# Performance work log

Hardware: AMD Instinct MI355X
Metric: run time of the kernel (lower is better)

The kernel has to match this reference:

```python
import jax, jax.numpy as jnp
import numpy as np

B, S, HID = 2, 1024, 2048
NH, NKV = 32, 8
HD = HID // NH          # 64
N_REP = NH // NKV       # 4
ROPE_BASE = 10000.0


def rope_tables(seq_len, dim):
    inv_freq = 1.0 / (ROPE_BASE ** (np.arange(0, dim, 2, dtype=np.float32) / dim))
    t = jnp.arange(seq_len, dtype=jnp.float32)
    freqs = jnp.outer(t, jnp.asarray(inv_freq))          # [S, HD/2]
    emb = jnp.concatenate([freqs, freqs], axis=-1)       # [S, HD]
    return jnp.cos(emb), jnp.sin(emb)


def rotate_half(x):
    half = x.shape[-1] // 2
    return jnp.concatenate([-x[..., half:], x[..., :half]], axis=-1)


def setup_inputs() -> dict:
    key = jax.random.key(0)
    k1, k2, k3, k4, k5 = jax.random.split(key, 5)
    hidden_states = jax.random.normal(k1, (B, S, HID), dtype=jnp.float32)
    position_ids = jnp.broadcast_to(jnp.arange(S, dtype=jnp.int32), (B, S))
    # additive causal mask [B,1,S,S]: 0 where allowed, large negative where masked
    neg = jnp.finfo(jnp.float32).min
    causal = jnp.tril(jnp.ones((S, S), dtype=bool))
    attention_mask = jnp.where(causal, 0.0, neg)[None, None].astype(jnp.float32)
    attention_mask = jnp.broadcast_to(attention_mask, (B, 1, S, S))
    scale = 0.02
    Wq = jax.random.normal(k2, (HID, NH * HD), dtype=jnp.float32) * scale
    Wk = jax.random.normal(k3, (HID, NKV * HD), dtype=jnp.float32) * scale
    Wv = jax.random.normal(k4, (HID, NKV * HD), dtype=jnp.float32) * scale
    Wo = jax.random.normal(k5, (HID, HID), dtype=jnp.float32) * scale
    return {"hidden_states": hidden_states, "position_ids": position_ids,
            "attention_mask": attention_mask, "Wq": Wq, "Wk": Wk, "Wv": Wv, "Wo": Wo}


def reference(hidden_states, position_ids, attention_mask, Wq, Wk, Wv, Wo):
    b, s, _ = hidden_states.shape
    q = (hidden_states @ Wq).reshape(b, s, NH, HD).transpose(0, 2, 1, 3)    # [b,H,s,d]
    k = (hidden_states @ Wk).reshape(b, s, NKV, HD).transpose(0, 2, 1, 3)   # [b,kv,s,d]
    v = (hidden_states @ Wv).reshape(b, s, NKV, HD).transpose(0, 2, 1, 3)

    cos_t, sin_t = rope_tables(s, HD)                    # [s, d]
    cos = cos_t[position_ids][:, None]                   # [b,1,s,d]
    sin = sin_t[position_ids][:, None]
    q = q * cos + rotate_half(q) * sin
    k = k * cos + rotate_half(k) * sin

    # GQA: repeat each kv head N_REP times along the head axis
    k = jnp.repeat(k, N_REP, axis=1)                     # [b,H,s,d]
    v = jnp.repeat(v, N_REP, axis=1)

    scale = 1.0 / jnp.sqrt(jnp.asarray(HD, dtype=q.dtype))
    scores = jnp.einsum('bhqd,bhkd->bhqk', q, k) * scale
    scores = scores + attention_mask
    scores = jnp.maximum(scores, jnp.finfo(scores.dtype).min)
    w = jax.nn.softmax(scores, axis=-1)
    out = jnp.einsum('bhqk,bhkd->bhqd', w, v)            # [b,H,s,d]
    out = out.transpose(0, 2, 1, 3).reshape(b, s, HID)
    return out @ Wo
```

## Files before the change

### kernel.cpp

```cpp
#include <hip/hip_runtime.h>
#include <hip/hip_bf16.h>
#include <math.h>

constexpr int BB   = 2;
constexpr int SS   = 1024;
constexpr int HID  = 2048;
constexpr int NH   = 32;
constexpr int NKV  = 8;
constexpr int HD   = 64;
constexpr int M    = BB * SS;
constexpr int NQKV = 3072;

typedef __attribute__((ext_vector_type(8))) short bf8v;
typedef __attribute__((ext_vector_type(4))) float f4v;

static __device__ __forceinline__ unsigned short f2b(float x) {
  __hip_bfloat16 h = __float2bfloat16(x);
  return *reinterpret_cast<unsigned short*>(&h);
}
static __device__ __forceinline__ void gload16(void* lds, const void* g) {
  __builtin_amdgcn_global_load_lds(
      (const __attribute__((address_space(1))) void*)g,
      (__attribute__((address_space(3))) void*)lds, 16, 0, 0);
}

__global__ __launch_bounds__(256) void prepAll(
    const float* __restrict__ Wq, const float* __restrict__ Wk,
    const float* __restrict__ Wv, const float* __restrict__ Wo,
    const float* __restrict__ hidden, const int* __restrict__ pos_ids,
    unsigned short* __restrict__ WqkvT, unsigned short* __restrict__ WoT,
    unsigned short* __restrict__ Xb, float2* __restrict__ tab) {
  const int z = blockIdx.z;
  const int t = threadIdx.x;

  if (z == 4) {
    const int idx = blockIdx.y * 32 + blockIdx.x;
    if ((t & 127) < 32) {
      const int m = idx * 2 + (t >> 7);
      const int j = t & 31;
      const float pos = (float)pos_ids[m];
      const float ang = pos * exp2f(-(float)j * (13.287712379549449f / 32.0f));
      float sn, cs;
      sincosf(ang, &sn, &cs);
      tab[(size_t)m * 32 + j] = make_float2(cs, sn);
    }
    return;
  }
  if (z == 5) {
    const size_t base = ((size_t)(blockIdx.y * 32 + blockIdx.x)) * 4096;
#pragma unroll
    for (int it = 0; it < 2; ++it) {
      const size_t i = base + it * 2048 + t * 8;
      const float4 v0 = *(const float4*)(hidden + i);
      const float4 v1 = *(const float4*)(hidden + i + 4);
      unsigned short o[8] = {f2b(v0.x), f2b(v0.y), f2b(v0.z), f2b(v0.w),
                             f2b(v1.x), f2b(v1.y), f2b(v1.z), f2b(v1.w)};
      *(bf8v*)(Xb + i) = *(bf8v*)o;
    }
    return;
  }

  const float* src;
  unsigned short* dst;
  int C;
  if (z == 0)      { src = Wq; dst = WqkvT;                      C = 2048; }
  else if (z == 1) { src = Wk; dst = WqkvT + (size_t)2048 * HID; C = 512;  }
  else if (z == 2) { src = Wv; dst = WqkvT + (size_t)2560 * HID; C = 512;  }
  else             { src = Wo; dst = WoT;                        C = 2048; }

  const int r0 = blockIdx.y * 64, c0 = blockIdx.x * 64;
  if (c0 >= C) return;
  __shared__ float T[64][65];
  {
    const int r  = t >> 2;
    const int c4 = (t & 3) * 16;
    const float* sp = src + (size_t)(r0 + r) * C + c0 + c4;
    *(float4*)&T[r][c4 + 0]  = *(const float4*)(sp + 0);
    *(float4*)&T[r][c4 + 4]  = *(const float4*)(sp + 4);
    *(float4*)&T[r][c4 + 8]  = *(const float4*)(sp + 8);
    *(float4*)&T[r][c4 + 12] = *(const float4*)(sp + 12);
  }
  __syncthreads();
  {
    const int c  = t >> 2;
    const int rr = (t & 3) * 16;
    unsigned short o[16];
#pragma unroll
    for (int i = 0; i < 16; ++i) o[i] = f2b(T[rr + i][c]);
    unsigned short* dp = dst + (size_t)(c0 + c) * HID + r0 + rr;
    *(bf8v*)dp       = *(bf8v*)&o[0];
    *(bf8v*)(dp + 8) = *(bf8v*)&o[8];
  }
}


__global__ __launch_bounds__(512) void gemm_qkv(
    const unsigned short* __restrict__ A, const unsigned short* __restrict__ Bt,
    const float2* __restrict__ tab,
    unsigned short* __restrict__ Qb, unsigned short* __restrict__ Kb,
    unsigned short* __restrict__ Vt) {
  __shared__ unsigned short As[4][64 * 32];
  __shared__ unsigned short Bs[4][128 * 32];
  const int t  = threadIdx.x;
  const int w  = t >> 6, l = t & 63;
  const int lr = l & 15, lg = l >> 4;
  const int wr = w >> 1, wc = w & 1;
  const int bm = blockIdx.y * 64, bn = blockIdx.x * 128;

  f4v acc[4] = {};

  const unsigned short* Ablk = A  + (size_t)bm * HID;
  const unsigned short* Bblk = Bt + (size_t)bn * HID;
  const int srow = l >> 2;
  const int scol = (((l & 3) ^ ((srow >> 1) & 3)) * 8);
  const int rsl  = (lg ^ ((lr >> 1) & 3)) * 8;

  auto stageSS = [&](int u) {
    const int b0 = (u & 1) * 2;
    const int k0 = u * 64;
    if (w < 4) {
      gload16(&As[b0][(w * 16) * 32],     Ablk + (size_t)(w * 16 + srow) * HID + k0 + scol);
      gload16(&As[b0 + 1][(w * 16) * 32], Ablk + (size_t)(w * 16 + srow) * HID + k0 + 32 + scol);
      gload16(&Bs[b0][(w * 16) * 32],     Bblk + (size_t)(w * 16 + srow) * HID + k0 + scol);
      gload16(&Bs[b0 + 1][(w * 16) * 32], Bblk + (size_t)(w * 16 + srow) * HID + k0 + 32 + scol);
    } else {
      gload16(&Bs[b0][(w * 16) * 32],     Bblk + (size_t)(w * 16 + srow) * HID + k0 + scol);
      gload16(&Bs[b0 + 1][(w * 16) * 32], Bblk + (size_t)(w * 16 + srow) * HID + k0 + 32 + scol);
    }
  };

  const int nss = HID / 64;
  stageSS(0);
  asm volatile("s_waitcnt vmcnt(0)" ::: "memory");
  __builtin_amdgcn_s_barrier();

  const int aoff = (wr * 16 + lr) * 32 + rsl;
  const int boff = (wc * 64 + lr) * 32 + rsl;
  for (int u = 0; u < nss; ++u) {
    if (u + 1 < nss) stageSS(u + 1);
    const int b0 = (u & 1) * 2;

#pragma unroll
    for (int hlf = 0; hlf < 2; ++hlf) {
      const int cb = b0 + hlf;
      bf8v aF = *(const bf8v*)&As[cb][aoff];
      bf8v bF[4];
#pragma unroll
      for (int j = 0; j < 4; ++j)
        bF[j] = *(const bf8v*)&Bs[cb][boff + j * 512];
      __builtin_amdgcn_s_setprio(1);
#pragma unroll
      for (int ni = 0; ni < 4; ++ni)
        acc[ni] = __builtin_amdgcn_mfma_f32_16x16x32_bf16(aF, bF[ni], acc[ni], 0, 0, 0);
      __builtin_amdgcn_s_setprio(0);
    }

    asm volatile("s_waitcnt vmcnt(0)" ::: "memory");
    __builtin_amdgcn_s_barrier();
  }

  const int row0 = bm + wr * 16;
  const int colHead = bn + wc * 64;
  int mode, hh;
  if (colHead < 2048)      { mode = 0; hh = colHead >> 6;          }
  else if (colHead < 2560) { mode = 1; hh = (colHead - 2048) >> 6; }
  else                     { mode = 2; hh = (colHead - 2560) >> 6; }

#pragma unroll
  for (int r = 0; r < 4; ++r) {
    const int rowg = row0 + lg * 4 + r;
    const int bI = rowg >> 10, s = rowg & (SS - 1);
    if (mode == 2) {
      unsigned short* base = Vt + ((size_t)(bI * NKV + hh) * 64) * SS + s;
#pragma unroll
      for (int ni = 0; ni < 4; ++ni)
        base[(size_t)(ni * 16 + lr) * SS] = f2b(acc[ni][r]);
    } else {
      unsigned short* dst = (mode == 0)
          ? Qb + ((size_t)(bI * NH  + hh) * SS + s) * 64
          : Kb + ((size_t)(bI * NKV + hh) * SS + s) * 64;
      const float2 cs_lo = tab[(size_t)rowg * 32 + lr];
      const float2 cs_hi = tab[(size_t)rowg * 32 + 16 + lr];
#pragma unroll
      for (int ni = 0; ni < 4; ++ni) {
        const float2 cs = (ni & 1) ? cs_hi : cs_lo;
        const float x   = acc[ni][r];
        const float prt = acc[ni ^ 2][r];
        const float rh  = (ni < 2) ? -prt : prt;
        float v = x * cs.x + rh * cs.y;
        if (mode == 0) v *= 0.125f;
        dst[ni * 16 + lr] = f2b(v);
      }
    }
  }
}

__global__ __launch_bounds__(512) void gemm_bf16(
    const unsigned short* __restrict__ A, const unsigned short* __restrict__ Bt,
    float* __restrict__ C, int Ndim) {
  __shared__ unsigned short As[4][64 * 32];
  __shared__ unsigned short Bs[4][128 * 32];
  const int t  = threadIdx.x;
  const int w  = t >> 6, l = t & 63;
  const int lr = l & 15, lg = l >> 4;
  const int wr = w >> 1, wc = w & 1;
  const int bm = blockIdx.y * 64, bn = blockIdx.x * 128;

  f4v acc[4] = {};

  const unsigned short* Ablk = A  + (size_t)bm * HID;
  const unsigned short* Bblk = Bt + (size_t)bn * HID;
  const int srow = l >> 2;
  const int scol = (((l & 3) ^ ((srow >> 1) & 3)) * 8);
  const int rsl  = (lg ^ ((lr >> 1) & 3)) * 8;

  auto stageSS = [&](int u) {
    const int b0 = (u & 1) * 2;
    const int k0 = u * 64;
    if (w < 4) {
      gload16(&As[b0][(w * 16) * 32],     Ablk + (size_t)(w * 16 + srow) * HID + k0 + scol);
      gload16(&As[b0 + 1][(w * 16) * 32], Ablk + (size_t)(w * 16 + srow) * HID + k0 + 32 + scol);
      gload16(&Bs[b0][(w * 16) * 32],     Bblk + (size_t)(w * 16 + srow) * HID + k0 + scol);
      gload16(&Bs[b0 + 1][(w * 16) * 32], Bblk + (size_t)(w * 16 + srow) * HID + k0 + 32 + scol);
    } else {
      gload16(&Bs[b0][(w * 16) * 32],     Bblk + (size_t)(w * 16 + srow) * HID + k0 + scol);
      gload16(&Bs[b0 + 1][(w * 16) * 32], Bblk + (size_t)(w * 16 + srow) * HID + k0 + 32 + scol);
    }
  };

  const int nss = HID / 64;
  stageSS(0);
  asm volatile("s_waitcnt vmcnt(0)" ::: "memory");
  __builtin_amdgcn_s_barrier();

  const int aoff = (wr * 16 + lr) * 32 + rsl;
  const int boff = (wc * 64 + lr) * 32 + rsl;
  for (int u = 0; u < nss; ++u) {
    if (u + 1 < nss) stageSS(u + 1);
    const int b0 = (u & 1) * 2;

#pragma unroll
    for (int hlf = 0; hlf < 2; ++hlf) {
      const int cb = b0 + hlf;
      bf8v aF = *(const bf8v*)&As[cb][aoff];
      bf8v bF[4];
#pragma unroll
      for (int j = 0; j < 4; ++j)
        bF[j] = *(const bf8v*)&Bs[cb][boff + j * 512];
      __builtin_amdgcn_s_setprio(1);
#pragma unroll
      for (int ni = 0; ni < 4; ++ni)
        acc[ni] = __builtin_amdgcn_mfma_f32_16x16x32_bf16(aF, bF[ni], acc[ni], 0, 0, 0);
      __builtin_amdgcn_s_setprio(0);
    }

    asm volatile("s_waitcnt vmcnt(0)" ::: "memory");
    __builtin_amdgcn_s_barrier();
  }

  const int row0 = bm + wr * 16;
  const int col0 = bn + wc * 64;
#pragma unroll
  for (int r = 0; r < 4; ++r) {
    const size_t rowoff = (size_t)(row0 + lg * 4 + r) * Ndim;
#pragma unroll
    for (int ni = 0; ni < 4; ++ni)
      C[rowoff + col0 + ni * 16 + lr] = acc[ni][r];
  }
}

__global__ __launch_bounds__(128) void attn_mfma(
    const unsigned short* __restrict__ Qb, const unsigned short* __restrict__ Kb,
    const unsigned short* __restrict__ Vt, unsigned short* __restrict__ attn) {
  const int xb = blockIdx.x;
  const int h = blockIdx.y, b = blockIdx.z;
  const int kv = h >> 2;
  const int w  = threadIdx.x >> 6;
  const int l  = threadIdx.x & 63;
  const int lr = l & 15;
  const int lg = l >> 4;
  const int t  = threadIdx.x;

  __shared__ unsigned short VT[64][72];
  __shared__ unsigned short PL[2][16][72];

  const unsigned short* Kp = Kb + ((size_t)((b * NKV + kv) * SS)) * 64;
  const unsigned short* Vp = Vt + ((size_t)((b * NKV + kv) * 64)) * SS;

  const int vd  = t >> 1;
  const int vso = (t & 1) * 32;

  for (int half = 0; half < 2; ++half) {
    const int qt = half ? (31 - xb) : xb;
    const int qbase = qt * 32;
    const int qW = qbase + w * 16;
    const unsigned short* Qp = Qb + ((size_t)((b * NH + h) * SS + qW)) * 64;
    bf8v aQ0 = *(const bf8v*)(Qp + (size_t)lr * 64 + lg * 8);
    bf8v aQ1 = *(const bf8v*)(Qp + (size_t)lr * 64 + 32 + lg * 8);

    f4v o[4] = {{0,0,0,0},{0,0,0,0},{0,0,0,0},{0,0,0,0}};
    float lsumL[4] = {0.f, 0.f, 0.f, 0.f};

    bf8v kc[8];
#pragma unroll
    for (int c = 0; c < 4; ++c) {
      const unsigned short* kr = Kp + (size_t)(c * 16 + lr) * 64 + lg * 8;
      kc[2 * c]     = *(const bf8v*)(kr);
      kc[2 * c + 1] = *(const bf8v*)(kr + 32);
    }

    for (int kvb = 0; kvb < qbase + 32; kvb += 64) {
      __syncthreads();
      const unsigned short* vp = Vp + (size_t)vd * SS + kvb + vso;
      const bf8v v0 = *(const bf8v*)(vp);
      const bf8v v1 = *(const bf8v*)(vp + 8);
      const bf8v v2 = *(const bf8v*)(vp + 16);
      const bf8v v3 = *(const bf8v*)(vp + 24);

      f4v sc[4] = {{0,0,0,0},{0,0,0,0},{0,0,0,0},{0,0,0,0}};
      __builtin_amdgcn_s_setprio(1);
#pragma unroll
      for (int c = 0; c < 4; ++c) {
        sc[c] = __builtin_amdgcn_mfma_f32_16x16x32_bf16(aQ0, kc[2 * c],     sc[c], 0, 0, 0);
        sc[c] = __builtin_amdgcn_mfma_f32_16x16x32_bf16(aQ1, kc[2 * c + 1], sc[c], 0, 0, 0);
      }
      __builtin_amdgcn_s_setprio(0);

      if (kvb + 64 < qbase + 32) {
#pragma unroll
        for (int c = 0; c < 4; ++c) {
          const unsigned short* kr = Kp + (size_t)(kvb + 64 + c * 16 + lr) * 64 + lg * 8;
          kc[2 * c]     = *(const bf8v*)(kr);
          kc[2 * c + 1] = *(const bf8v*)(kr + 32);
        }
      }

#pragma unroll
      for (int r = 0; r < 4; ++r) {
        const int qrow = qW + lg * 4 + r;
        float ps = 0.f;
        unsigned short pb[4];
#pragma unroll
        for (int c = 0; c < 4; ++c) {
          const float s = ((kvb + c * 16 + lr) > qrow) ? -INFINITY : sc[c][r];
          const float p = __expf(s);
          ps += p;
          pb[c] = f2b(p);
        }
        lsumL[r] += ps;
#pragma unroll
        for (int c = 0; c < 4; ++c) PL[w][lg * 4 + r][c * 16 + lr] = pb[c];
      }

      *(bf8v*)&VT[vd][vso]      = v0;
      *(bf8v*)&VT[vd][vso + 8]  = v1;
      *(bf8v*)&VT[vd][vso + 16] = v2;
      *(bf8v*)&VT[vd][vso + 24] = v3;

      __syncthreads();

      bf8v aP0 = *(const bf8v*)&PL[w][lr][lg * 8];
      bf8v aP1 = *(const bf8v*)&PL[w][lr][32 + lg * 8];
      __builtin_amdgcn_s_setprio(1);
#pragma unroll
      for (int n = 0; n < 4; ++n) {
        bf8v bV0 = *(const bf8v*)&VT[n * 16 + lr][lg * 8];
        bf8v bV1 = *(const bf8v*)&VT[n * 16 + lr][32 + lg * 8];
        o[n] = __builtin_amdgcn_mfma_f32_16x16x32_bf16(aP0, bV0, o[n], 0, 0, 0);
        o[n] = __builtin_amdgcn_mfma_f32_16x16x32_bf16(aP1, bV1, o[n], 0, 0, 0);
      }
      __builtin_amdgcn_s_setprio(0);
    }

#pragma unroll
    for (int r = 0; r < 4; ++r) {
      float ls = lsumL[r];
      ls += __shfl_xor(ls, 1);
      ls += __shfl_xor(ls, 2);
      ls += __shfl_xor(ls, 4);
      ls += __shfl_xor(ls, 8);
      const float inv = 1.0f / ls;
      const int row = qW + lg * 4 + r;
      unsigned short* dst = attn + (size_t)(b * SS + row) * HID + h * 64;
#pragma unroll
      for (int n = 0; n < 4; ++n) dst[n * 16 + lr] = f2b(o[n][r] * inv);
    }
  }
}

extern "C" void kernel_launch(void* const* d_in, const int* in_sizes, int n_in,
                              void* d_out, int out_size, void* d_ws, size_t ws_size,
                              hipStream_t stream) {
  const float* hidden = (const float*)d_in[0];
  const int*   pos    = (const int*)d_in[1];
  const float* Wq = (const float*)d_in[3];
  const float* Wk = (const float*)d_in[4];
  const float* Wv = (const float*)d_in[5];
  const float* Wo = (const float*)d_in[6];
  float* out = (float*)d_out;

  char* ws = (char*)d_ws;
  unsigned short* WqkvT = (unsigned short*)(ws);
  unsigned short* WoT   = (unsigned short*)(ws + 12582912);
  unsigned short* Xb    = (unsigned short*)(ws + 20971520);
  unsigned short* attnb = Xb;
  unsigned short* Qb    = (unsigned short*)(ws + 29360128);
  unsigned short* Kb    = (unsigned short*)(ws + 37748736);
  unsigned short* Vt    = (unsigned short*)(ws + 39845888);
  float2*         tab   = (float2*)(ws + 41943040);

  dim3 blk(256);

  prepAll<<<dim3(32, 32, 6), blk, 0, stream>>>(Wq, Wk, Wv, Wo, hidden, pos,
                                               WqkvT, WoT, Xb, tab);

  gemm_qkv<<<dim3(NQKV / 128, M / 64), dim3(512), 0, stream>>>(Xb, WqkvT, tab, Qb, Kb, Vt);

  attn_mfma<<<dim3(16, NH, BB), dim3(128), 0, stream>>>(Qb, Kb, Vt, attnb);

  gemm_bf16<<<dim3(HID / 128, M / 64), dim3(512), 0, stream>>>(attnb, WoT, out, HID);
}
```

Measured before the change: 132.0 us.

## Compute transposed attention tiles to keep P and V in registers, removing block syncs

Swaps the MFMA operand order so scores come out transposed (key rows by query columns). This lets the softmax probabilities be redistributed with wave shuffles instead of an LDS round-trip, and lets V fragments load straight from global memory into registers with prefetch. Both __syncthreads per KV block and the VT/PL shared buffers are removed. The cost is more cross-lane shuffles and register pressure, plus a small LDS transpose in the epilogue.

```diff
diff --git a/kernel.cpp b/kernel.cpp
--- a/kernel.cpp
+++ b/kernel.cpp
@@ -13,6 +13,7 @@
 
 typedef __attribute__((ext_vector_type(8))) short bf8v;
 typedef __attribute__((ext_vector_type(4))) float f4v;
+typedef __attribute__((ext_vector_type(4))) int   i4v;
 
 static __device__ __forceinline__ unsigned short f2b(float x) {
   __hip_bfloat16 h = __float2bfloat16(x);
@@ -279,16 +280,14 @@
   const int l  = threadIdx.x & 63;
   const int lr = l & 15;
   const int lg = l >> 4;
-  const int t  = threadIdx.x;
-
-  __shared__ unsigned short VT[64][72];
-  __shared__ unsigned short PL[2][16][72];
+
+  __shared__ float scr[2][16][68];
 
   const unsigned short* Kp = Kb + ((size_t)((b * NKV + kv) * SS)) * 64;
   const unsigned short* Vp = Vt + ((size_t)((b * NKV + kv) * 64)) * SS;
 
-  const int vd  = t >> 1;
-  const int vso = (t & 1) * 32;
+  const int src0 = (lg & 1) * 32 + lr;
+  const int src1 = src0 + 16;
 
   for (int half = 0; half < 2; ++half) {
     const int qt = half ? (31 - xb) : xb;
@@ -299,7 +298,9 @@
     bf8v aQ1 = *(const bf8v*)(Qp + (size_t)lr * 64 + 32 + lg * 8);
 
     f4v o[4] = {{0,0,0,0},{0,0,0,0},{0,0,0,0},{0,0,0,0}};
-    float lsumL[4] = {0.f, 0.f, 0.f, 0.f};
+    float lsum = 0.f;
+
+    const int nkv = (qbase + 32 + 63) >> 6;
 
     bf8v kc[8];
 #pragma unroll
@@ -308,25 +309,26 @@
       kc[2 * c]     = *(const bf8v*)(kr);
       kc[2 * c + 1] = *(const bf8v*)(kr + 32);
     }
-
-    for (int kvb = 0; kvb < qbase + 32; kvb += 64) {
-      __syncthreads();
-      const unsigned short* vp = Vp + (size_t)vd * SS + kvb + vso;
-      const bf8v v0 = *(const bf8v*)(vp);
-      const bf8v v1 = *(const bf8v*)(vp + 8);
-      const bf8v v2 = *(const bf8v*)(vp + 16);
-      const bf8v v3 = *(const bf8v*)(vp + 24);
+    bf8v vA[8];
+#pragma unroll
+    for (int n = 0; n < 4; ++n)
+#pragma unroll
+      for (int ks = 0; ks < 2; ++ks)
+        vA[n * 2 + ks] = *(const bf8v*)(Vp + (size_t)(n * 16 + lr) * SS + ks * 32 + lg * 8);
+
+    for (int j = 0; j < nkv; ++j) {
+      const int kvb = j * 64;
 
       f4v sc[4] = {{0,0,0,0},{0,0,0,0},{0,0,0,0},{0,0,0,0}};
       __builtin_amdgcn_s_setprio(1);
 #pragma unroll
       for (int c = 0; c < 4; ++c) {
-        sc[c] = __builtin_amdgcn_mfma_f32_16x16x32_bf16(aQ0, kc[2 * c],     sc[c], 0, 0, 0);
-        sc[c] = __builtin_amdgcn_mfma_f32_16x16x32_bf16(aQ1, kc[2 * c + 1], sc[c], 0, 0, 0);
+        sc[c] = __builtin_amdgcn_mfma_f32_16x16x32_bf16(kc[2 * c],     aQ0, sc[c], 0, 0, 0);
+        sc[c] = __builtin_amdgcn_mfma_f32_16x16x32_bf16(kc[2 * c + 1], aQ1, sc[c], 0, 0, 0);
       }
       __builtin_amdgcn_s_setprio(0);
 
-      if (kvb + 64 < qbase + 32) {
+      if (j + 1 < nkv) {
 #pragma unroll
         for (int c = 0; c < 4; ++c) {
           const unsigned short* kr = Kp + (size_t)(kvb + 64 + c * 16 + lr) * 64 + lg * 8;
@@ -335,55 +337,66 @@
         }
       }
 
-#pragma unroll
-      for (int r = 0; r < 4; ++r) {
-        const int qrow = qW + lg * 4 + r;
-        float ps = 0.f;
-        unsigned short pb[4];
-#pragma unroll
-        for (int c = 0; c < 4; ++c) {
-          const float s = ((kvb + c * 16 + lr) > qrow) ? -INFINITY : sc[c][r];
-          const float p = __expf(s);
-          ps += p;
-          pb[c] = f2b(p);
-        }
-        lsumL[r] += ps;
-#pragma unroll
-        for (int c = 0; c < 4; ++c) PL[w][lg * 4 + r][c * 16 + lr] = pb[c];
-      }
-
-      *(bf8v*)&VT[vd][vso]      = v0;
-      *(bf8v*)&VT[vd][vso + 8]  = v1;
-      *(bf8v*)&VT[vd][vso + 16] = v2;
-      *(bf8v*)&VT[vd][vso + 24] = v3;
-
-      __syncthreads();
-
-      bf8v aP0 = *(const bf8v*)&PL[w][lr][lg * 8];
-      bf8v aP1 = *(const bf8v*)&PL[w][lr][32 + lg * 8];
+      unsigned pk[4][2];
+      const int q = qW + lr;
+#pragma unroll
+      for (int c = 0; c < 4; ++c) {
+        const int kbase = kvb + c * 16 + lg * 4;
+        float p0 = (kbase + 0 > q) ? 0.f : __expf(sc[c][0]);
+        float p1 = (kbase + 1 > q) ? 0.f : __expf(sc[c][1]);
+        float p2 = (kbase + 2 > q) ? 0.f : __expf(sc[c][2]);
+        float p3 = (kbase + 3 > q) ? 0.f : __expf(sc[c][3]);
+        lsum += (p0 + p1) + (p2 + p3);
+        pk[c][0] = (unsigned)f2b(p0) | ((unsigned)f2b(p1) << 16);
+        pk[c][1] = (unsigned)f2b(p2) | ((unsigned)f2b(p3) << 16);
+      }
+
+      bf8v bP[2];
+#pragma unroll
+      for (int ks = 0; ks < 2; ++ks) {
+        const int c0 = 2 * ks, c1 = 2 * ks + 1;
+        int a0 = __shfl((int)pk[c0][0], src0), b0 = __shfl((int)pk[c1][0], src0);
+        int a1 = __shfl((int)pk[c0][1], src0), b1 = __shfl((int)pk[c1][1], src0);
+        int a2 = __shfl((int)pk[c0][0], src1), b2 = __shfl((int)pk[c1][0], src1);
+        int a3 = __shfl((int)pk[c0][1], src1), b3 = __shfl((int)pk[c1][1], src1);
+        const bool hi = (lg & 2);
+        i4v uu = { hi ? b0 : a0, hi ? b1 : a1, hi ? b2 : a2, hi ? b3 : a3 };
+        bP[ks] = *reinterpret_cast<bf8v*>(&uu);
+      }
+
       __builtin_amdgcn_s_setprio(1);
 #pragma unroll
       for (int n = 0; n < 4; ++n) {
-        bf8v bV0 = *(const bf8v*)&VT[n * 16 + lr][lg * 8];
-        bf8v bV1 = *(const bf8v*)&VT[n * 16 + lr][32 + lg * 8];
-        o[n] = __builtin_amdgcn_mfma_f32_16x16x32_bf16(aP0, bV0, o[n], 0, 0, 0);
-        o[n] = __builtin_amdgcn_mfma_f32_16x16x32_bf16(aP1, bV1, o[n], 0, 0, 0);
+        o[n] = __builtin_amdgcn_mfma_f32_16x16x32_bf16(vA[n * 2 + 0], bP[0], o[n], 0, 0, 0);
+        o[n] = __builtin_amdgcn_mfma_f32_16x16x32_bf16(vA[n * 2 + 1], bP[1], o[n], 0, 0, 0);
       }
       __builtin_amdgcn_s_setprio(0);
-    }
-
-#pragma unroll
-    for (int r = 0; r < 4; ++r) {
-      float ls = lsumL[r];
-      ls += __shfl_xor(ls, 1);
-      ls += __shfl_xor(ls, 2);
-      ls += __shfl_xor(ls, 4);
-      ls += __shfl_xor(ls, 8);
-      const float inv = 1.0f / ls;
-      const int row = qW + lg * 4 + r;
+
+      if (j + 1 < nkv) {
+#pragma unroll
+        for (int n = 0; n < 4; ++n)
+#pragma unroll
+          for (int ks = 0; ks < 2; ++ks)
+            vA[n * 2 + ks] = *(const bf8v*)(Vp + (size_t)(n * 16 + lr) * SS + kvb + 64 + ks * 32 + lg * 8);
+      }
+    }
+
+    lsum += __shfl_xor(lsum, 16);
+    lsum += __shfl_xor(lsum, 32);
+    const float inv = 1.0f / lsum;
+
+#pragma unroll
+    for (int n = 0; n < 4; ++n)
+#pragma unroll
+      for (int r = 0; r < 4; ++r)
+        scr[w][lr][n * 16 + lg * 4 + r] = o[n][r] * inv;
+#pragma unroll
+    for (int r2 = 0; r2 < 4; ++r2) {
+      const int row = qW + lg * 4 + r2;
       unsigned short* dst = attn + (size_t)(b * SS + row) * HID + h * 64;
 #pragma unroll
-      for (int n = 0; n < 4; ++n) dst[n * 16 + lr] = f2b(o[n][r] * inv);
+      for (int n = 0; n < 4; ++n)
+        dst[n * 16 + lr] = f2b(scr[w][lg * 4 + r2][n * 16 + lr]);
     }
   }
 }
```

Measured after the change: 151.9 us. +15.1%, slower.
